# Performance work log

Measured on AMD Instinct MI355X. Metric: run time of the kernel, lower is better.

Reference implementation:

```python
import jax, jax.numpy as jnp
import numpy as np

IN_C = 128
OUT_C = 128
MEM = 512
HID = MEM // 2  # 256, per ParameterGenerator hidden_channels = memory_size // 2
T = 8          # number of edge types (keys of edge_feas_dict)
N = 500_000


def setup_inputs() -> dict:
    key = jax.random.key(0)
    ks = jax.random.split(key, 16)
    s = 0.02
    inp = {
        "x": jax.random.normal(ks[0], (N, IN_C), dtype=jnp.float32),
        "type_vec": jax.random.randint(ks[1], (N,), 0, T),
        "edge_feas": jax.random.normal(ks[2], (T, MEM), dtype=jnp.float32),
        # weight_generator MLP: Linear(MEM,HID) -> ReLU -> Linear(HID,HID) -> ReLU -> Linear(HID, IN_C*OUT_C)
        "wg_w1": jax.random.normal(ks[3], (MEM, HID), dtype=jnp.float32) * s,
        "wg_b1": jnp.zeros((HID,), dtype=jnp.float32),
        "wg_w2": jax.random.normal(ks[4], (HID, HID), dtype=jnp.float32) * s,
        "wg_b2": jnp.zeros((HID,), dtype=jnp.float32),
        "wg_w3": jax.random.normal(ks[5], (HID, IN_C * OUT_C), dtype=jnp.float32) * s,
        "wg_b3": jnp.zeros((IN_C * OUT_C,), dtype=jnp.float32),
        # bias_generator MLP: Linear(MEM,HID) -> ReLU -> Linear(HID,HID) -> ReLU -> Linear(HID, OUT_C)
        "bg_w1": jax.random.normal(ks[6], (MEM, HID), dtype=jnp.float32) * s,
        "bg_b1": jnp.zeros((HID,), dtype=jnp.float32),
        "bg_w2": jax.random.normal(ks[7], (HID, HID), dtype=jnp.float32) * s,
        "bg_b2": jnp.zeros((HID,), dtype=jnp.float32),
        "bg_w3": jax.random.normal(ks[8], (HID, OUT_C), dtype=jnp.float32) * s,
        "bg_b3": jnp.zeros((OUT_C,), dtype=jnp.float32),
    }
    return inp


def _mlp(m, w1, b1, w2, b2, w3, b3):
    h = jax.nn.relu(m @ w1 + b1)
    h = jax.nn.relu(h @ w2 + b2)
    return h @ w3 + b3


def reference(x, type_vec, edge_feas,
              wg_w1, wg_b1, wg_w2, wg_b2, wg_w3, wg_b3,
              bg_w1, bg_b1, bg_w2, bg_b2, bg_w3, bg_b3):
    # Generate per-type weights [T, IN_C, OUT_C] and biases [T, OUT_C]
    W = _mlp(edge_feas, wg_w1, wg_b1, wg_w2, wg_b2, wg_w3, wg_b3).reshape(T, IN_C, OUT_C)
    B = _mlp(edge_feas, bg_w1, bg_b1, bg_w2, bg_b2, bg_w3, bg_b3)  # [T, OUT_C]
    # Masked per-type linear, scattered back: out[n] = x[n] @ W[type_vec[n]] + B[type_vec[n]]
    out = jnp.zeros((x.shape[0], OUT_C), dtype=x.dtype)
    for t in range(T):  # small fixed set of types
        yt = x @ W[t] + B[t]
        out = jnp.where((type_vec == t)[:, None], yt, out)
    return out
```

## Files before the change

### kernel.cpp

```cpp
#include <hip/hip_runtime.h>
#include <hip/hip_bf16.h>

#define NT 8
#define MEMC 512
#define HID 256
#define C 128

typedef __attribute__((ext_vector_type(8))) short short8;
typedef __attribute__((ext_vector_type(4))) float f32x4;

__device__ inline short f2bf(float f) {
    union { __hip_bfloat16 b; short s; } u;
    u.b = __float2bfloat16(f);
    return u.s;
}

__global__ __launch_bounds__(256) void k1_init_genh(
    const float* __restrict__ edge_feas,
    const float* __restrict__ wg_w1, const float* __restrict__ wg_b1,
    const float* __restrict__ wg_w2, const float* __restrict__ wg_b2,
    const float* __restrict__ bg_w1, const float* __restrict__ bg_b1,
    const float* __restrict__ bg_w2, const float* __restrict__ bg_b2,
    int* __restrict__ hist, int* __restrict__ cursor,
    int* __restrict__ idx, int idx_cap,
    float* __restrict__ h_wg, float* __restrict__ h_bg,
    int n_init_blocks)
{
    int b = blockIdx.x, tid = threadIdx.x;
    if (b < n_init_blocks) {
        int pos = b * 1024 + tid * 4;
        if (pos < idx_cap) *(int4*)(idx + pos) = make_int4(-1, -1, -1, -1);
        return;
    }
    if (b == n_init_blocks) {
        if (tid < NT) { hist[tid] = 0; cursor[tid * 16] = 0; }
        return;
    }
    int gb = b - n_init_blocks - 1;
    int t = gb & 7;
    int gen = gb >> 3;
    const float* w1 = gen ? bg_w1 : wg_w1;
    const float* b1 = gen ? bg_b1 : wg_b1;
    const float* w2 = gen ? bg_w2 : wg_w2;
    const float* b2 = gen ? bg_b2 : wg_b2;
    float* hout = gen ? h_bg : h_wg;

    __shared__ float m[MEMC];
    __shared__ float part[4][HID];
    __shared__ float h1[HID];
    m[tid]       = edge_feas[t * MEMC + tid];
    m[tid + 256] = edge_feas[t * MEMC + tid + 256];
    __syncthreads();

    int w = tid >> 6, l = tid & 63;
    {
        float ax = 0.f, ay = 0.f, az = 0.f, aw = 0.f;
        const float* wp = w1 + (size_t)(w * 128) * HID + 4 * l;
        #pragma unroll 8
        for (int k = 0; k < 128; ++k) {
            float4 v = *(const float4*)(wp + (size_t)k * HID);
            float mk = m[w * 128 + k];
            ax += mk * v.x; ay += mk * v.y; az += mk * v.z; aw += mk * v.w;
        }
        *(float4*)&part[w][4 * l] = make_float4(ax, ay, az, aw);
    }
    __syncthreads();
    {
        float s = part[0][tid] + part[1][tid] + part[2][tid] + part[3][tid] + b1[tid];
        h1[tid] = fmaxf(s, 0.f);
    }
    __syncthreads();
    {
        float ax = 0.f, ay = 0.f, az = 0.f, aw = 0.f;
        const float* wp = w2 + (size_t)(w * 64) * HID + 4 * l;
        #pragma unroll 8
        for (int k = 0; k < 64; ++k) {
            float4 v = *(const float4*)(wp + (size_t)k * HID);
            float hk = h1[w * 64 + k];
            ax += hk * v.x; ay += hk * v.y; az += hk * v.z; aw += hk * v.w;
        }
        *(float4*)&part[w][4 * l] = make_float4(ax, ay, az, aw);
    }
    __syncthreads();
    {
        float s = part[0][tid] + part[1][tid] + part[2][tid] + part[3][tid] + b2[tid];
        hout[t * HID + tid] = fmaxf(s, 0.f);
    }
}

__global__ __launch_bounds__(256) void k2_hist_genw(
    const int* __restrict__ type_vec, int N,
    const float* __restrict__ h_wg, const float* __restrict__ h_bg,
    const float* __restrict__ wg_w3, const float* __restrict__ wg_b3,
    const float* __restrict__ bg_w3, const float* __restrict__ bg_b3,
    int* __restrict__ hist, short* __restrict__ Wt, float* __restrict__ Bias,
    int n_hist_blocks)
{
    int b = blockIdx.x, tid = threadIdx.x;
    __shared__ float sh[2048];
    __shared__ float sp[2048];
    if (b < n_hist_blocks) {
        int lane = tid & 63, wv = tid >> 6;
        int start = b * 1024 + wv * 256;
        int cnt[NT];
        #pragma unroll
        for (int t = 0; t < NT; ++t) cnt[t] = 0;
        #pragma unroll
        for (int c = 0; c < 4; ++c) {
            int n = start + c * 64 + lane;
            int mt = (n < N) ? type_vec[n] : NT;
            #pragma unroll
            for (int t = 0; t < NT; ++t)
                cnt[t] += __popcll(__ballot(mt == t));
        }
        if (lane < NT) atomicAdd(&hist[lane], cnt[lane]);
        return;
    }
    int gb = b - n_hist_blocks;
    if (gb < 256) {
        for (int i = tid; i < 2048; i += 256) sh[i] = h_wg[i];
        __syncthreads();
        int cl = tid & 63, p = tid >> 6;
        int col = gb * 64 + cl;
        float acc[NT];
        #pragma unroll
        for (int t = 0; t < NT; ++t) acc[t] = 0.f;
        const float* wp = wg_w3 + (size_t)(p * 64) * (C * C) + col;
        #pragma unroll 8
        for (int j = 0; j < 64; ++j) {
            float v = wp[(size_t)j * (C * C)];
            #pragma unroll
            for (int t = 0; t < NT; ++t) acc[t] += sh[t * 256 + p * 64 + j] * v;
        }
        #pragma unroll
        for (int t = 0; t < NT; ++t) sp[p * 512 + t * 64 + cl] = acc[t];
        __syncthreads();
        #pragma unroll
        for (int r = 0; r < 2; ++r) {
            int o = tid + 256 * r;
            int t = o >> 6, c2 = o & 63;
            float s = sp[t * 64 + c2] + sp[512 + t * 64 + c2]
                    + sp[1024 + t * 64 + c2] + sp[1536 + t * 64 + c2]
                    + wg_b3[gb * 64 + c2];
            int flat = gb * 64 + c2;
            Wt[t * (C * C) + (flat & 127) * C + (flat >> 7)] = f2bf(s);
        }
        return;
    }
    for (int i = tid; i < 2048; i += 256) sh[i] = h_bg[i];
    __syncthreads();
    int cl = tid & 127, p = tid >> 7;
    float acc[NT];
    #pragma unroll
    for (int t = 0; t < NT; ++t) acc[t] = 0.f;
    const float* wp = bg_w3 + (size_t)(p * 128) * C + cl;
    #pragma unroll 8
    for (int j = 0; j < 128; ++j) {
        float v = wp[(size_t)j * C];
        #pragma unroll
        for (int t = 0; t < NT; ++t) acc[t] += sh[t * 256 + p * 128 + j] * v;
    }
    #pragma unroll
    for (int t = 0; t < NT; ++t) sp[p * 1024 + t * 128 + cl] = acc[t];
    __syncthreads();
    #pragma unroll
    for (int r = 0; r < 4; ++r) {
        int o = tid + 256 * r;
        int t = o >> 7, c2 = o & 127;
        Bias[t * C + c2] = sp[t * 128 + c2] + sp[1024 + t * 128 + c2] + bg_b3[c2];
    }
}

__global__ __launch_bounds__(256) void k4_scatter(
    const int* __restrict__ type_vec, int N,
    const int* __restrict__ hist, int* __restrict__ cursor,
    int* __restrict__ idx)
{
    int b = blockIdx.x, tid = threadIdx.x;
    int seg[NT];
    {
        int s = 0;
        #pragma unroll
        for (int t = 0; t < NT; ++t) { seg[t] = s; s += ((hist[t] + 127) >> 7) << 7; }
    }
    int lane = tid & 63;
    int wave = b * 4 + (tid >> 6);
    int start = wave * 1024;
    if (start >= N) return;

    int cnt[NT];
    #pragma unroll
    for (int t = 0; t < NT; ++t) cnt[t] = 0;
    for (int c = 0; c < 16; ++c) {
        int n = start + c * 64 + lane;
        int mt = (n < N) ? type_vec[n] : NT;
        #pragma unroll
        for (int t = 0; t < NT; ++t)
            cnt[t] += __popcll(__ballot(mt == t));
    }
    int base = 0;
    if (lane < NT) base = atomicAdd(&cursor[lane * 16], cnt[lane]);
    int run[NT];
    #pragma unroll
    for (int t = 0; t < NT; ++t) run[t] = seg[t] + __shfl(base, t, 64);
    unsigned long long below = (1ULL << lane) - 1ULL;
    for (int c = 0; c < 16; ++c) {
        int n = start + c * 64 + lane;
        int mt = (n < N) ? type_vec[n] : NT;
        int mypos = 0;
        #pragma unroll
        for (int t = 0; t < NT; ++t) {
            unsigned long long msk = __ballot(mt == t);
            if (mt == t) mypos = run[t] + __popcll(msk & below);
            run[t] += __popcll(msk);
        }
        if (n < N) idx[mypos] = n;
    }
}

__global__ __launch_bounds__(512, 6) void k5_gemm(
    const float* __restrict__ x, const int* __restrict__ idx,
    const short* __restrict__ Wt, const float* __restrict__ Bias,
    const int* __restrict__ hist, float* __restrict__ out)
{
    __shared__ short Bs[C * C];
    int tid = threadIdx.x;
    int lane = tid & 63, w = tid >> 6;
    int m16 = lane & 15, quad = lane >> 4;
    int block_base = blockIdx.x * 128;

    int seg[NT + 1];
    {
        int s = 0;
        #pragma unroll
        for (int t = 0; t < NT; ++t) { seg[t] = s; s += ((hist[t] + 127) >> 7) << 7; }
        seg[NT] = s;
    }
    if (block_base >= seg[NT]) return;
    int t = 0;
    #pragma unroll
    for (int i = 1; i < NT; ++i)
        if (block_base >= seg[i]) t = i;

    int row0 = block_base + 16 * w;
    int node_a = idx[row0 + m16];

    short8 bstg[4];
    {
        const short* wsrc = Wt + t * (C * C);
        #pragma unroll
        for (int i = 0; i < 4; ++i)
            bstg[i] = *(const short8*)(wsrc + (size_t)(i * 512 + tid) * 8);
    }

    float4 a0[4], a1[4];
    {
        const float* xr = x + (size_t)(node_a < 0 ? 0 : node_a) * C + quad * 8;
        #pragma unroll
        for (int kk = 0; kk < 4; ++kk) {
            a0[kk] = *(const float4*)(xr + kk * 32);
            a1[kk] = *(const float4*)(xr + kk * 32 + 4);
        }
    }

    {
        #pragma unroll
        for (int i = 0; i < 4; ++i) {
            int s = i * 512 + tid;
            int row = s >> 4, sl = s & 15;
            *(short8*)((char*)Bs + row * 256 + ((sl ^ (row & 15)) << 4)) = bstg[i];
        }
    }

    __syncthreads();

    short8 af[4];
    #pragma unroll
    for (int kk = 0; kk < 4; ++kk) {
        short8 sv;
        sv[0] = f2bf(a0[kk].x); sv[1] = f2bf(a0[kk].y);
        sv[2] = f2bf(a0[kk].z); sv[3] = f2bf(a0[kk].w);
        sv[4] = f2bf(a1[kk].x); sv[5] = f2bf(a1[kk].y);
        sv[6] = f2bf(a1[kk].z); sv[7] = f2bf(a1[kk].w);
        af[kk] = sv;
    }
    if (node_a < 0) {
        #pragma unroll
        for (int kk = 0; kk < 4; ++kk)
            af[kk] = (short8){0, 0, 0, 0, 0, 0, 0, 0};
    }

    f32x4 acc[8];
    #pragma unroll
    for (int i = 0; i < 8; ++i) acc[i] = (f32x4){0.f, 0.f, 0.f, 0.f};

    {
        const char* bbase = (const char*)Bs + m16 * 256;
        #pragma unroll
        for (int kk = 0; kk < 4; ++kk) {
            int cswz = (((kk * 4 + quad) ^ m16) << 4);
            #pragma unroll
            for (int ni = 0; ni < 8; ++ni) {
                short8 bf = *(const short8*)(bbase + (ni << 12) + cswz);
                acc[ni] = __builtin_amdgcn_mfma_f32_16x16x32_bf16(af[kk], bf, acc[ni], 0, 0, 0);
            }
        }
    }

    int node_c[4];
    #pragma unroll
    for (int r = 0; r < 4; ++r) node_c[r] = idx[row0 + quad * 4 + r];

    #pragma unroll
    for (int ni = 0; ni < 8; ++ni) {
        float bv = Bias[t * C + ni * 16 + m16];
        #pragma unroll
        for (int r = 0; r < 4; ++r) {
            if (node_c[r] >= 0)
                out[(size_t)node_c[r] * C + ni * 16 + m16] = acc[ni][r] + bv;
        }
    }
}

extern "C" void kernel_launch(void* const* d_in, const int* in_sizes, int n_in,
                              void* d_out, int out_size, void* d_ws, size_t ws_size,
                              hipStream_t stream)
{
    const float* x         = (const float*)d_in[0];
    const int*   type_vec  = (const int*)d_in[1];
    const float* edge_feas = (const float*)d_in[2];
    const float* wg_w1 = (const float*)d_in[3];
    const float* wg_b1 = (const float*)d_in[4];
    const float* wg_w2 = (const float*)d_in[5];
    const float* wg_b2 = (const float*)d_in[6];
    const float* wg_w3 = (const float*)d_in[7];
    const float* wg_b3 = (const float*)d_in[8];
    const float* bg_w1 = (const float*)d_in[9];
    const float* bg_b1 = (const float*)d_in[10];
    const float* bg_w2 = (const float*)d_in[11];
    const float* bg_b2 = (const float*)d_in[12];
    const float* bg_w3 = (const float*)d_in[13];
    const float* bg_b3 = (const float*)d_in[14];
    float* out = (float*)d_out;
    int N = in_sizes[1];

    char* ws = (char*)d_ws;
    int*   hist   = (int*)(ws + 0);
    int*   cursor = (int*)(ws + 128);
    float* h_wg   = (float*)(ws + 1024);
    float* h_bg   = (float*)(ws + 9216);
    float* Bias   = (float*)(ws + 17408);
    short* Wt     = (short*)(ws + 21504);
    int*   idx    = (int*)(ws + 283648);

    int nblk128 = (N + 127) / 128;
    int idx_cap = (nblk128 + 8) * 128;
    int n_init  = (idx_cap + 1023) / 1024;
    int n_hist  = (N + 1023) / 1024;
    int n_scat  = (n_hist + 3) / 4;

    k1_init_genh<<<n_init + 17, 256, 0, stream>>>(
        edge_feas, wg_w1, wg_b1, wg_w2, wg_b2, bg_w1, bg_b1, bg_w2, bg_b2,
        hist, cursor, idx, idx_cap, h_wg, h_bg, n_init);

    k2_hist_genw<<<n_hist + 257, 256, 0, stream>>>(
        type_vec, N, h_wg, h_bg, wg_w3, wg_b3, bg_w3, bg_b3,
        hist, Wt, Bias, n_hist);

    k4_scatter<<<n_scat, 256, 0, stream>>>(
        type_vec, N, hist, cursor, idx);

    k5_gemm<<<nblk128 + 8, 512, 0, stream>>>(x, idx, Wt, Bias, hist, out);
}
```

Before: 554.4 us.

## Drop idx init pass, use per-segment bounds, block-level scatter atomics

Removes the -1 fill of the index buffer. The GEMM kernel instead derives validity from each type segment's histogram bound, so padding rows are masked by position rather than by sentinel values. The scatter kernel now gives each block 1024 elements, with four waves combining their counts in shared memory so a single atomic per type per block replaces per-wave atomics. The GEMM also hoists the bias and output-index loads earlier and relaxes the occupancy hint in launch bounds. Reads of uninitialised idx entries are clamped, but they still happen.

```diff
diff --git a/kernel.cpp b/kernel.cpp
--- a/kernel.cpp
+++ b/kernel.cpp
@@ -22,21 +22,14 @@
     const float* __restrict__ bg_w1, const float* __restrict__ bg_b1,
     const float* __restrict__ bg_w2, const float* __restrict__ bg_b2,
     int* __restrict__ hist, int* __restrict__ cursor,
-    int* __restrict__ idx, int idx_cap,
-    float* __restrict__ h_wg, float* __restrict__ h_bg,
-    int n_init_blocks)
+    float* __restrict__ h_wg, float* __restrict__ h_bg)
 {
     int b = blockIdx.x, tid = threadIdx.x;
-    if (b < n_init_blocks) {
-        int pos = b * 1024 + tid * 4;
-        if (pos < idx_cap) *(int4*)(idx + pos) = make_int4(-1, -1, -1, -1);
-        return;
-    }
-    if (b == n_init_blocks) {
+    if (b == 0) {
         if (tid < NT) { hist[tid] = 0; cursor[tid * 16] = 0; }
         return;
     }
-    int gb = b - n_init_blocks - 1;
+    int gb = b - 1;
     int t = gb & 7;
     int gen = gb >> 3;
     const float* w1 = gen ? bg_w1 : wg_w1;
@@ -177,34 +170,46 @@
     int* __restrict__ idx)
 {
     int b = blockIdx.x, tid = threadIdx.x;
+    int lane = tid & 63, wv = tid >> 6;
+    __shared__ int pb[4][NT];
+
     int seg[NT];
     {
         int s = 0;
         #pragma unroll
         for (int t = 0; t < NT; ++t) { seg[t] = s; s += ((hist[t] + 127) >> 7) << 7; }
     }
-    int lane = tid & 63;
-    int wave = b * 4 + (tid >> 6);
-    int start = wave * 1024;
-    if (start >= N) return;
+    int start = b * 1024 + wv * 256;
 
     int cnt[NT];
     #pragma unroll
     for (int t = 0; t < NT; ++t) cnt[t] = 0;
-    for (int c = 0; c < 16; ++c) {
+    #pragma unroll
+    for (int c = 0; c < 4; ++c) {
         int n = start + c * 64 + lane;
         int mt = (n < N) ? type_vec[n] : NT;
         #pragma unroll
         for (int t = 0; t < NT; ++t)
             cnt[t] += __popcll(__ballot(mt == t));
     }
-    int base = 0;
-    if (lane < NT) base = atomicAdd(&cursor[lane * 16], cnt[lane]);
+    if (lane < NT) pb[wv][lane] = cnt[lane];
+    __syncthreads();
+    if (tid < NT) {
+        int s0 = pb[0][tid], s1 = pb[1][tid], s2 = pb[2][tid], s3 = pb[3][tid];
+        int base = atomicAdd(&cursor[tid * 16], s0 + s1 + s2 + s3);
+        pb[0][tid] = base;
+        pb[1][tid] = base + s0;
+        pb[2][tid] = base + s0 + s1;
+        pb[3][tid] = base + s0 + s1 + s2;
+    }
+    __syncthreads();
     int run[NT];
     #pragma unroll
-    for (int t = 0; t < NT; ++t) run[t] = seg[t] + __shfl(base, t, 64);
+    for (int t = 0; t < NT; ++t) run[t] = seg[t] + pb[wv][t];
+
     unsigned long long below = (1ULL << lane) - 1ULL;
-    for (int c = 0; c < 16; ++c) {
+    #pragma unroll
+    for (int c = 0; c < 4; ++c) {
         int n = start + c * 64 + lane;
         int mt = (n < N) ? type_vec[n] : NT;
         int mypos = 0;
@@ -218,7 +223,7 @@
     }
 }
 
-__global__ __launch_bounds__(512, 6) void k5_gemm(
+__global__ __launch_bounds__(512, 4) void k5_gemm(
     const float* __restrict__ x, const int* __restrict__ idx,
     const short* __restrict__ Wt, const float* __restrict__ Bias,
     const int* __restrict__ hist, float* __restrict__ out)
@@ -229,11 +234,15 @@
     int m16 = lane & 15, quad = lane >> 4;
     int block_base = blockIdx.x * 128;
 
-    int seg[NT + 1];
+    int seg[NT + 1], harr[NT];
     {
         int s = 0;
         #pragma unroll
-        for (int t = 0; t < NT; ++t) { seg[t] = s; s += ((hist[t] + 127) >> 7) << 7; }
+        for (int t = 0; t < NT; ++t) {
+            harr[t] = hist[t];
+            seg[t] = s;
+            s += ((harr[t] + 127) >> 7) << 7;
+        }
         seg[NT] = s;
     }
     if (block_base >= seg[NT]) return;
@@ -241,9 +250,16 @@
     #pragma unroll
     for (int i = 1; i < NT; ++i)
         if (block_base >= seg[i]) t = i;
+    int vlim = 0;
+    #pragma unroll
+    for (int i = 0; i < NT; ++i)
+        if (i == t) vlim = seg[i] + harr[i];
 
     int row0 = block_base + 16 * w;
-    int node_a = idx[row0 + m16];
+    int rowA = row0 + m16;
+    bool validA = rowA < vlim;
+    int node_a = idx[rowA];
+    int na = validA ? node_a : 0;
 
     short8 bstg[4];
     {
@@ -255,13 +271,25 @@
 
     float4 a0[4], a1[4];
     {
-        const float* xr = x + (size_t)(node_a < 0 ? 0 : node_a) * C + quad * 8;
+        const float* xr = x + (size_t)na * C + quad * 8;
         #pragma unroll
         for (int kk = 0; kk < 4; ++kk) {
             a0[kk] = *(const float4*)(xr + kk * 32);
             a1[kk] = *(const float4*)(xr + kk * 32 + 4);
         }
     }
+
+    int node_c[4];
+    bool valid_c[4];
+    #pragma unroll
+    for (int r = 0; r < 4; ++r) {
+        int rowC = row0 + quad * 4 + r;
+        valid_c[r] = rowC < vlim;
+        node_c[r] = idx[rowC];
+    }
+    float bv[8];
+    #pragma unroll
+    for (int ni = 0; ni < 8; ++ni) bv[ni] = Bias[t * C + ni * 16 + m16];
 
     {
         #pragma unroll
@@ -284,7 +312,7 @@
         sv[6] = f2bf(a1[kk].z); sv[7] = f2bf(a1[kk].w);
         af[kk] = sv;
     }
-    if (node_a < 0) {
+    if (!validA) {
         #pragma unroll
         for (int kk = 0; kk < 4; ++kk)
             af[kk] = (short8){0, 0, 0, 0, 0, 0, 0, 0};
@@ -307,17 +335,12 @@
         }
     }
 
-    int node_c[4];
-    #pragma unroll
-    for (int r = 0; r < 4; ++r) node_c[r] = idx[row0 + quad * 4 + r];
-
     #pragma unroll
     for (int ni = 0; ni < 8; ++ni) {
-        float bv = Bias[t * C + ni * 16 + m16];
         #pragma unroll
         for (int r = 0; r < 4; ++r) {
-            if (node_c[r] >= 0)
-                out[(size_t)node_c[r] * C + ni * 16 + m16] = acc[ni][r] + bv;
+            if (valid_c[r])
+                out[(size_t)node_c[r] * C + ni * 16 + m16] = acc[ni][r] + bv[ni];
         }
     }
 }
@@ -354,20 +377,17 @@
     int*   idx    = (int*)(ws + 283648);
 
     int nblk128 = (N + 127) / 128;
-    int idx_cap = (nblk128 + 8) * 128;
-    int n_init  = (idx_cap + 1023) / 1024;
     int n_hist  = (N + 1023) / 1024;
-    int n_scat  = (n_hist + 3) / 4;
-
-    k1_init_genh<<<n_init + 17, 256, 0, stream>>>(
+
+    k1_init_genh<<<17, 256, 0, stream>>>(
         edge_feas, wg_w1, wg_b1, wg_w2, wg_b2, bg_w1, bg_b1, bg_w2, bg_b2,
-        hist, cursor, idx, idx_cap, h_wg, h_bg, n_init);
+        hist, cursor, h_wg, h_bg);
 
     k2_hist_genw<<<n_hist + 257, 256, 0, stream>>>(
         type_vec, N, h_wg, h_bg, wg_w3, wg_b3, bg_w3, bg_b3,
         hist, Wt, Bias, n_hist);
 
-    k4_scatter<<<n_scat, 256, 0, stream>>>(
+    k4_scatter<<<n_hist, 256, 0, stream>>>(
         type_vec, N, hist, cursor, idx);
 
     k5_gemm<<<nblk128 + 8, 512, 0, stream>>>(x, idx, Wt, Bias, hist, out);
```

Measured after the change: 538.2 us. 2.9% less time.
